# Optimization experiments

Hardware: AMD Instinct MI355X
Metric: run time of the kernel (lower is better)

## Reference

```python
import jax, jax.numpy as jnp
import numpy as np
from jax import lax

BN_EPS = 1e-5
DIST_EPS = 1e-8

def _three_nn_interpolate(xyz1, xyz2, points2):
    # squared pairwise distances: (B, N, S)
    d2 = (jnp.sum(xyz1 ** 2, -1)[:, :, None]
          + jnp.sum(xyz2 ** 2, -1)[:, None, :]
          - 2.0 * jnp.einsum('bnd,bsd->bns', xyz1, xyz2))
    neg_d, idx = lax.top_k(-d2, 3)            # 3 nearest -> (B, N, 3)
    dist = -neg_d
    recip = 1.0 / (dist + DIST_EPS)
    weight = recip / jnp.sum(recip, -1, keepdims=True)   # (B, N, 3)
    gathered = jax.vmap(lambda p, i: p[i])(points2, idx)  # (B, N, 3, C2)
    return jnp.einsum('bnkc,bnk->bnc', gathered, weight)

def _conv_bn_relu(x, w, g, b):
    # x: (B, N, Cin); 1x1 conv == matmul; BatchNorm1d over (B, N) per channel (training stats)
    y = jnp.einsum('bnc,oc->bno', x, w)
    mu = jnp.mean(y, axis=(0, 1))
    var = jnp.mean((y - mu) ** 2, axis=(0, 1))
    yn = (y - mu) * lax.rsqrt(var + BN_EPS)
    return jax.nn.relu(yn * g + b)

def setup_inputs() -> dict:
    key = jax.random.key(0)
    ks = jax.random.split(key, 6)
    B, N, S, C1, C2 = 16, 4096, 1024, 256, 256
    return {
        'xyz1': jax.random.normal(ks[0], (B, N, 3), jnp.float32),
        'xyz2': jax.random.normal(ks[1], (B, S, 3), jnp.float32),
        'points1': jax.random.normal(ks[2], (B, N, C1), jnp.float32),
        'points2': jax.random.normal(ks[3], (B, S, C2), jnp.float32),
        'w1': jax.random.normal(ks[4], (256, C1 + C2), jnp.float32) * 0.04,
        'g1': jnp.ones((256,), jnp.float32),
        'b1': jnp.zeros((256,), jnp.float32),
        'w2': jax.random.normal(ks[5], (256, 256), jnp.float32) * 0.06,
        'g2': jnp.ones((256,), jnp.float32),
        'b2': jnp.zeros((256,), jnp.float32),
    }

def reference(xyz1, xyz2, points1, points2, w1, g1, b1, w2, g2, b2):
    interp = _three_nn_interpolate(xyz1, xyz2, points2)    # (B, N, C2)
    feats = jnp.concatenate([points1, interp], axis=-1)    # (B, N, C1+C2)
    h = _conv_bn_relu(feats, w1, g1, b1)
    out = _conv_bn_relu(h, w2, g2, b2)
    return out                                              # (B, N, 256)
```

## Files before the change

### kernel.cpp

```cpp
#include <hip/hip_runtime.h>
#include <stdint.h>

typedef unsigned short ushort_t;
typedef __bf16 bf16x8 __attribute__((ext_vector_type(8)));
typedef float f32x4 __attribute__((ext_vector_type(4)));
typedef unsigned short ushort8 __attribute__((ext_vector_type(8)));
typedef unsigned short ushort4_t __attribute__((ext_vector_type(4)));

#define DEV static __device__ __forceinline__

DEV unsigned short f2bf(float f) {
    union { float f; unsigned int i; } v; v.f = f;
    unsigned int u = v.i;
    return (unsigned short)((u + 0x7fffu + ((u >> 16) & 1u)) >> 16);
}
DEV float bf2f(unsigned short u) {
    union { unsigned int i; float f; } v; v.i = ((unsigned int)u) << 16; return v.f;
}
DEV bf16x8 u2b(ushort8 u) { union { ushort8 u; bf16x8 b; } x; x.u = u; return x.b; }

__global__ __launch_bounds__(256) void prep_kernel(
    const float* __restrict__ w1, const float* __restrict__ w2,
    const float* __restrict__ points2,
    ushort_t* __restrict__ w1b, ushort_t* __restrict__ w2b,
    ushort_t* __restrict__ p2b, float* __restrict__ stats)
{
    const int bx = blockIdx.x;
    if (bx < 512) {
        int i = bx * 256 + threadIdx.x;
        w1b[i] = f2bf(w1[i]);
    } else if (bx < 768) {
        int i = (bx - 512) * 256 + threadIdx.x;
        w2b[i] = f2bf(w2[i]);
    } else if (bx < 4864) {
        int i = ((bx - 768) * 256 + threadIdx.x) * 4;
        float4 v = *(const float4*)(points2 + i);
        ushort4_t o;
        o[0] = f2bf(v.x); o[1] = f2bf(v.y); o[2] = f2bf(v.z); o[3] = f2bf(v.w);
        *(ushort4_t*)(p2b + i) = o;
    } else {
        int i = threadIdx.x * 8;
        *(float4*)(stats + i)     = make_float4(0.f, 0.f, 0.f, 0.f);
        *(float4*)(stats + i + 4) = make_float4(0.f, 0.f, 0.f, 0.f);
    }
}

__global__ __launch_bounds__(256) void knn_kernel(
    const float* __restrict__ xyz1, const float* __restrict__ xyz2,
    int* __restrict__ idx_out, float* __restrict__ w_out)
{
    __shared__ float4 P[1024];
    __shared__ float mD[24][32];
    __shared__ int   mI[24][32];
    const int b = blockIdx.y;
    const int tid = threadIdx.x;
    for (int s = tid; s < 1024; s += 256) {
        const float* p = xyz2 + ((size_t)b * 1024 + s) * 3;
        float x = p[0], y = p[1], z = p[2];
        float pp = __fadd_rn(__fadd_rn(__fmul_rn(x, x), __fmul_rn(y, y)), __fmul_rn(z, z));
        P[s] = make_float4(x, y, z, pp);
    }
    __syncthreads();
    const int ql = tid & 31;
    const int chunk = tid >> 5;
    const int n = blockIdx.x * 32 + ql;
    const float* q = xyz1 + ((size_t)b * 4096 + n) * 3;
    float qx = q[0], qy = q[1], qz = q[2];
    float qq = __fadd_rn(__fadd_rn(__fmul_rn(qx, qx), __fmul_rn(qy, qy)), __fmul_rn(qz, qz));
    float d0 = 1e30f, d1 = 1e30f, d2 = 1e30f;
    int i0 = 0, i1 = 0, i2 = 0;
    const int s0 = chunk * 128;
#pragma unroll 4
    for (int s = s0; s < s0 + 128; ++s) {
        float4 p = P[s];
        float dot = __fadd_rn(__fadd_rn(__fmul_rn(qx, p.x), __fmul_rn(qy, p.y)), __fmul_rn(qz, p.z));
        float d = __fsub_rn(__fadd_rn(qq, p.w), __fmul_rn(2.0f, dot));
        if (d < d2) {
            if (d < d1) {
                d2 = d1; i2 = i1;
                if (d < d0) { d1 = d0; i1 = i0; d0 = d; i0 = s; }
                else        { d1 = d;  i1 = s; }
            } else { d2 = d; i2 = s; }
        }
    }
    mD[chunk * 3 + 0][ql] = d0; mI[chunk * 3 + 0][ql] = i0;
    mD[chunk * 3 + 1][ql] = d1; mI[chunk * 3 + 1][ql] = i1;
    mD[chunk * 3 + 2][ql] = d2; mI[chunk * 3 + 2][ql] = i2;
    __syncthreads();
    if (tid < 32) {
        float e0 = 1e30f, e1 = 1e30f, e2 = 1e30f;
        int j0 = 0, j1 = 0, j2 = 0;
#pragma unroll
        for (int c = 0; c < 24; ++c) {
            float d = mD[c][ql]; int i = mI[c][ql];
            if (d < e2) {
                if (d < e1) {
                    e2 = e1; j2 = j1;
                    if (d < e0) { e1 = e0; j1 = j0; e0 = d; j0 = i; }
                    else        { e1 = d;  j1 = i; }
                } else { e2 = d; j2 = i; }
            }
        }
        float r0 = 1.0f / (e0 + 1e-8f);
        float r1 = 1.0f / (e1 + 1e-8f);
        float r2 = 1.0f / (e2 + 1e-8f);
        float rs = __fadd_rn(__fadd_rn(r0, r1), r2);
        size_t o = ((size_t)b * 4096 + n) * 3;
        idx_out[o + 0] = j0; idx_out[o + 1] = j1; idx_out[o + 2] = j2;
        w_out[o + 0] = r0 / rs; w_out[o + 1] = r1 / rs; w_out[o + 2] = r2 / rs;
    }
}

DEV void cvt8(const float4& u0, const float4& u1, ushort8& hv) {
    hv[0] = f2bf(u0.x); hv[1] = f2bf(u0.y); hv[2] = f2bf(u0.z); hv[3] = f2bf(u0.w);
    hv[4] = f2bf(u1.x); hv[5] = f2bf(u1.y); hv[6] = f2bf(u1.z); hv[7] = f2bf(u1.w);
}

__global__ __launch_bounds__(1024, 4) void gemm1_kernel(
    const float* __restrict__ p1, const ushort_t* __restrict__ p2b,
    const int* __restrict__ idx, const float* __restrict__ wgt,
    const ushort_t* __restrict__ w1b, ushort_t* __restrict__ y,
    float* __restrict__ sums, float* __restrict__ sqs)
{
    __shared__ __align__(16) char smem[133120];
    ushort_t* Bs = (ushort_t*)smem;
    const int tid = threadIdx.x;
    const int wave = tid >> 6, lane = tid & 63;
    const int frl = lane & 15, fq = lane >> 4;
    const int bid = blockIdx.x;
    const int xcd = bid & 7;
    const int j6 = bid >> 3;
    const int batch = xcd * 2 + (j6 >> 5);
    const int wblk = j6 & 31;
    const int panel = batch * 16 + (wblk >> 1), nb = wblk & 1;
    const int m0 = panel * 256;

    {
        const int c = tid >> 3, qq = tid & 7;
        const ushort_t* src = w1b + (size_t)(nb * 128 + c) * 512;
        ushort_t* dst = Bs + c * 520;
#pragma unroll
        for (int s = 0; s < 8; ++s) {
            int off = qq * 8 + s * 64;
            *(ushort8*)(dst + off) = *(const ushort8*)(src + off);
        }
    }

    f32x4 acc[8];
#pragma unroll
    for (int j = 0; j < 8; ++j) acc[j] = f32x4{0.0f, 0.0f, 0.0f, 0.0f};

    const int row0 = m0 + wave * 16 + frl;
    const size_t io = (size_t)row0 * 3;
    const float iw0 = wgt[io], iw1 = wgt[io + 1], iw2 = wgt[io + 2];
    const ushort_t* pb = p2b + (size_t)(row0 >> 12) * (1024 * 256);
    const ushort_t* gp0 = pb + (size_t)idx[io] * 256 + fq * 8;
    const ushort_t* gp1 = pb + (size_t)idx[io + 1] * 256 + fq * 8;
    const ushort_t* gp2 = pb + (size_t)idx[io + 2] * 256 + fq * 8;

    __syncthreads();

    bf16x8 afb[2], bfb[2][8];

#define G1_LOADA(buf, kc) {                                                        \
    if ((kc) < 8) {                                                                \
        const float4* g = (const float4*)(p1 + (size_t)row0 * 256                  \
                                          + (kc) * 32 + fq * 8);                   \
        float4 u0 = g[0], u1 = g[1];                                               \
        ushort8 hv; cvt8(u0, u1, hv);                                              \
        buf = u2b(hv);                                                             \
    } else {                                                                       \
        ushort8 ga = *(const ushort8*)(gp0 + ((kc) - 8) * 32);                     \
        ushort8 gb = *(const ushort8*)(gp1 + ((kc) - 8) * 32);                     \
        ushort8 gc = *(const ushort8*)(gp2 + ((kc) - 8) * 32);                     \
        ushort8 hv;                                                                \
        _Pragma("unroll")                                                          \
        for (int e = 0; e < 8; ++e) {                                              \
            float av = __fmul_rn(iw0, bf2f(ga[e]));                                \
            av = fmaf(iw1, bf2f(gb[e]), av);                                       \
            av = fmaf(iw2, bf2f(gc[e]), av);                                       \
            hv[e] = f2bf(av);                                                      \
        }                                                                          \
        buf = u2b(hv);                                                             \
    } }
#define G1_LOADB(buf, kc) { _Pragma("unroll")                                      \
    for (int j = 0; j < 8; ++j)                                                    \
        buf[j] = *(const bf16x8*)(Bs + (j * 16 + frl) * 520 + (kc) * 32 + fq * 8); }

    G1_LOADA(afb[0], 0); G1_LOADB(bfb[0], 0);
#pragma unroll
    for (int kc = 0; kc < 16; ++kc) {
        const int cur = kc & 1, nxt = cur ^ 1;
        if (kc < 15) { G1_LOADA(afb[nxt], kc + 1); G1_LOADB(bfb[nxt], kc + 1); }
#pragma unroll
        for (int j = 0; j < 8; ++j)
            acc[j] = __builtin_amdgcn_mfma_f32_16x16x32_bf16(afb[cur], bfb[cur][j], acc[j], 0, 0, 0);
    }

    float ps[8], pq[8];
#pragma unroll
    for (int j = 0; j < 8; ++j) {
        const int colg = nb * 128 + j * 16 + frl;
        float s = 0.f, q = 0.f;
#pragma unroll
        for (int rr = 0; rr < 4; ++rr) {
            ushort_t hb = f2bf(acc[j][rr]);
            float v = bf2f(hb);
            y[(size_t)(m0 + wave * 16 + fq * 4 + rr) * 256 + colg] = hb;
            s += v; q = fmaf(v, v, q);
        }
        s += __shfl_xor(s, 16); s += __shfl_xor(s, 32);
        q += __shfl_xor(q, 16); q += __shfl_xor(q, 32);
        ps[j] = s; pq[j] = q;
    }
    __syncthreads();
    float* scrS = (float*)smem;
    float* scrQ = (float*)(smem + 8192);
    if (fq == 0) {
#pragma unroll
        for (int j = 0; j < 8; ++j) {
            scrS[wave * 128 + j * 16 + frl] = ps[j];
            scrQ[wave * 128 + j * 16 + frl] = pq[j];
        }
    }
    __syncthreads();
    if (tid < 128) {
        float s = 0.f, q = 0.f;
#pragma unroll
        for (int w = 0; w < 16; ++w) { s += scrS[w * 128 + tid]; q += scrQ[w * 128 + tid]; }
        atomicAdd(&sums[nb * 128 + tid], s);
        atomicAdd(&sqs[nb * 128 + tid], q);
    }
}

__global__ __launch_bounds__(512, 2) void gemm2_kernel(
    const ushort_t* __restrict__ y1, const ushort_t* __restrict__ w2b,
    const float* __restrict__ sums1, const float* __restrict__ sqs1,
    const float* __restrict__ g1, const float* __restrict__ b1,
    ushort_t* __restrict__ y2, float* __restrict__ sums, float* __restrict__ sqs)
{
    __shared__ __align__(16) char smem[137216];
    ushort_t* As = (ushort_t*)smem;
    ushort_t* Bs = (ushort_t*)(smem + 67584);
    float* sAv = (float*)(smem + 135168);
    float* sCv = (float*)(smem + 136192);
    const int tid = threadIdx.x;
    const int wave = tid >> 6, lane = tid & 63;
    const int frl = lane & 15, fq = lane >> 4;
    const int panel = blockIdx.x >> 1, nb = blockIdx.x & 1;
    const int m0 = panel * 128;

    if (tid < 256) {
        const float inv_n = 1.0f / 65536.0f;
        float mu = sums1[tid] * inv_n;
        float var = fmaf(-mu, mu, sqs1[tid] * inv_n);
        float is = 1.0f / sqrtf(var + 1e-5f);
        float aa = g1[tid] * is;
        sAv[tid] = aa;
        sCv[tid] = fmaf(-mu, aa, b1[tid]);
    }
    __syncthreads();

    {
        const int r = tid >> 2, qq = tid & 3;
        const ushort_t* srcA = y1 + (size_t)(m0 + r) * 256;
        ushort_t* dstA = As + r * 264;
        const ushort_t* srcB = w2b + (size_t)(nb * 128 + r) * 256;
        ushort_t* dstB = Bs + r * 264;
#pragma unroll
        for (int s = 0; s < 8; ++s) {
            int off = qq * 8 + s * 32;
            ushort8 raw = *(const ushort8*)(srcA + off);
            ushort8 hv;
#pragma unroll
            for (int e = 0; e < 8; ++e) {
                float v = bf2f(raw[e]);
                hv[e] = f2bf(fmaxf(fmaf(v, sAv[off + e], sCv[off + e]), 0.0f));
            }
            *(ushort8*)(dstA + off) = hv;
            *(ushort8*)(dstB + off) = *(const ushort8*)(srcB + off);
        }
    }

    f32x4 acc[2][4];
#pragma unroll
    for (int i = 0; i < 2; ++i)
#pragma unroll
        for (int j = 0; j < 4; ++j) acc[i][j] = f32x4{0.0f, 0.0f, 0.0f, 0.0f};

    __syncthreads();

    const int rg = (wave & 3) * 32, cg = (wave >> 2) * 64;
    bf16x8 afb[2][2], bfb[2][4];

#define G2_LOADA(buf, kc) { _Pragma("unroll")                                      \
    for (int i = 0; i < 2; ++i)                                                    \
        buf[i] = *(const bf16x8*)(As + (rg + i * 16 + frl) * 264 + (kc) * 32 + fq * 8); }
#define G2_LOADB(buf, kc) { _Pragma("unroll")                                      \
    for (int j = 0; j < 4; ++j)                                                    \
        buf[j] = *(const bf16x8*)(Bs + (cg + j * 16 + frl) * 264 + (kc) * 32 + fq * 8); }

    G2_LOADA(afb[0], 0); G2_LOADB(bfb[0], 0);
#pragma unroll
    for (int kc = 0; kc < 8; ++kc) {
        const int cur = kc & 1, nxt = cur ^ 1;
        if (kc < 7) { G2_LOADA(afb[nxt], kc + 1); G2_LOADB(bfb[nxt], kc + 1); }
#pragma unroll
        for (int i = 0; i < 2; ++i)
#pragma unroll
            for (int j = 0; j < 4; ++j)
                acc[i][j] = __builtin_amdgcn_mfma_f32_16x16x32_bf16(afb[cur][i], bfb[cur][j], acc[i][j], 0, 0, 0);
    }

    float ps[4], pq[4];
#pragma unroll
    for (int j = 0; j < 4; ++j) {
        const int colg = nb * 128 + cg + j * 16 + frl;
        float s = 0.f, q = 0.f;
#pragma unroll
        for (int i = 0; i < 2; ++i)
#pragma unroll
            for (int rr = 0; rr < 4; ++rr) {
                ushort_t hb = f2bf(acc[i][j][rr]);
                float v = bf2f(hb);
                y2[(size_t)(m0 + rg + i * 16 + fq * 4 + rr) * 256 + colg] = hb;
                s += v; q = fmaf(v, v, q);
            }
        s += __shfl_xor(s, 16); s += __shfl_xor(s, 32);
        q += __shfl_xor(q, 16); q += __shfl_xor(q, 32);
        ps[j] = s; pq[j] = q;
    }
    __syncthreads();
    float* scrS = (float*)smem;
    float* scrQ = (float*)(smem + 2048);
    if (fq == 0) {
#pragma unroll
        for (int j = 0; j < 4; ++j) {
            scrS[wave * 64 + j * 16 + frl] = ps[j];
            scrQ[wave * 64 + j * 16 + frl] = pq[j];
        }
    }
    __syncthreads();
    if (tid < 128) {
        const int g = tid >> 6, cw = tid & 63;
        float s = 0.f, q = 0.f;
#pragma unroll
        for (int k = 0; k < 4; ++k) {
            s += scrS[(g * 4 + k) * 64 + cw];
            q += scrQ[(g * 4 + k) * 64 + cw];
        }
        atomicAdd(&sums[nb * 128 + g * 64 + cw], s);
        atomicAdd(&sqs[nb * 128 + g * 64 + cw], q);
    }
}

__global__ __launch_bounds__(256) void apply_kernel(
    const ushort_t* __restrict__ y2,
    const float* __restrict__ sums2, const float* __restrict__ sqs2,
    const float* __restrict__ g2, const float* __restrict__ b2,
    float* __restrict__ out)
{
    __shared__ float sA[256], sC[256];
    {
        const int ch2 = threadIdx.x;
        const float inv_n = 1.0f / 65536.0f;
        float mu = sums2[ch2] * inv_n;
        float var = fmaf(-mu, mu, sqs2[ch2] * inv_n);
        float is = 1.0f / sqrtf(var + 1e-5f);
        float aa = g2[ch2] * is;
        sA[ch2] = aa;
        sC[ch2] = fmaf(-mu, aa, b2[ch2]);
    }
    __syncthreads();
    const size_t i = ((size_t)blockIdx.x * 256 + threadIdx.x) * 8;
    const int ch = (int)(i & 255);
    ushort8 raw = *(const ushort8*)(y2 + i);
    float4 o0, o1;
    const float4 a0 = *(const float4*)(sA + ch), a1v = *(const float4*)(sA + ch + 4);
    const float4 c0 = *(const float4*)(sC + ch), c1v = *(const float4*)(sC + ch + 4);
    o0.x = fmaxf(fmaf(bf2f(raw[0]), a0.x, c0.x), 0.0f);
    o0.y = fmaxf(fmaf(bf2f(raw[1]), a0.y, c0.y), 0.0f);
    o0.z = fmaxf(fmaf(bf2f(raw[2]), a0.z, c0.z), 0.0f);
    o0.w = fmaxf(fmaf(bf2f(raw[3]), a0.w, c0.w), 0.0f);
    o1.x = fmaxf(fmaf(bf2f(raw[4]), a1v.x, c1v.x), 0.0f);
    o1.y = fmaxf(fmaf(bf2f(raw[5]), a1v.y, c1v.y), 0.0f);
    o1.z = fmaxf(fmaf(bf2f(raw[6]), a1v.z, c1v.z), 0.0f);
    o1.w = fmaxf(fmaf(bf2f(raw[7]), a1v.w, c1v.w), 0.0f);
    *(float4*)(out + i) = o0;
    *(float4*)(out + i + 4) = o1;
}

extern "C" void kernel_launch(void* const* d_in, const int* in_sizes, int n_in,
                              void* d_out, int out_size, void* d_ws, size_t ws_size,
                              hipStream_t stream)
{
    const float* xyz1    = (const float*)d_in[0];
    const float* xyz2    = (const float*)d_in[1];
    const float* points1 = (const float*)d_in[2];
    const float* points2 = (const float*)d_in[3];
    const float* w1      = (const float*)d_in[4];
    const float* g1      = (const float*)d_in[5];
    const float* b1      = (const float*)d_in[6];
    const float* w2      = (const float*)d_in[7];
    const float* g2      = (const float*)d_in[8];
    const float* b2      = (const float*)d_in[9];
    float* out = (float*)d_out;

    char* ws = (char*)d_ws;
    float* sums1 = (float*)(ws + 0);
    float* sqs1  = (float*)(ws + 1024);
    float* sums2 = (float*)(ws + 4096);
    float* sqs2  = (float*)(ws + 5120);
    ushort_t* w1b = (ushort_t*)(ws + (64u << 10));
    ushort_t* w2b = (ushort_t*)(ws + (320u << 10));
    ushort_t* p2b = (ushort_t*)(ws + (1u << 20));
    int*   idx   = (int*)(ws + (10u << 20));
    float* wgt   = (float*)(ws + (11u << 20));
    ushort_t* y2b = (ushort_t*)(ws + (12u << 20));
    ushort_t* y1  = (ushort_t*)(ws + (44u << 20));

    prep_kernel<<<dim3(4865), 256, 0, stream>>>(w1, w2, points2, w1b, w2b, p2b, (float*)ws);
    knn_kernel<<<dim3(128, 16), 256, 0, stream>>>(xyz1, xyz2, idx, wgt);
    gemm1_kernel<<<dim3(512), 1024, 0, stream>>>(points1, p2b, idx, wgt, w1b, y1, sums1, sqs1);
    gemm2_kernel<<<dim3(1024), 512, 0, stream>>>(y1, w2b, sums1, sqs1, g1, b1, y2b, sums2, sqs2);
    apply_kernel<<<dim3(8192), 256, 0, stream>>>(y2b, sums2, sqs2, g2, b2, out);
}
```

Before: 272.8 us.

## Load gemm2 A operand directly from global into registers, halving LDS footprint

gemm2 no longer stages the normalized y1 tile in shared memory. Each wave now owns 16 rows and all 128 columns, and reads its A fragments straight from global memory, applying BN1+ReLU in registers. Shared memory use drops to about 68KB and the launch bounds hint moves to 4 blocks per CU, aiming at higher occupancy and one fewer staging pass. The cost is that B fragments are now read by every wave for 8 column tiles, and A reads are uncoalesced row slices from global memory.

```diff
diff --git a/kernel.cpp b/kernel.cpp
--- a/kernel.cpp
+++ b/kernel.cpp
@@ -233,17 +233,16 @@
     }
 }
 
-__global__ __launch_bounds__(512, 2) void gemm2_kernel(
+__global__ __launch_bounds__(512, 4) void gemm2_kernel(
     const ushort_t* __restrict__ y1, const ushort_t* __restrict__ w2b,
     const float* __restrict__ sums1, const float* __restrict__ sqs1,
     const float* __restrict__ g1, const float* __restrict__ b1,
     ushort_t* __restrict__ y2, float* __restrict__ sums, float* __restrict__ sqs)
 {
-    __shared__ __align__(16) char smem[137216];
-    ushort_t* As = (ushort_t*)smem;
-    ushort_t* Bs = (ushort_t*)(smem + 67584);
-    float* sAv = (float*)(smem + 135168);
-    float* sCv = (float*)(smem + 136192);
+    __shared__ __align__(16) char smem[69632];
+    ushort_t* Bs = (ushort_t*)smem;
+    float* sAv = (float*)(smem + 67584);
+    float* sCv = (float*)(smem + 68608);
     const int tid = threadIdx.x;
     const int wave = tid >> 6, lane = tid & 63;
     const int frl = lane & 15, fq = lane >> 4;
@@ -259,46 +258,41 @@
         sAv[tid] = aa;
         sCv[tid] = fmaf(-mu, aa, b1[tid]);
     }
-    __syncthreads();
 
     {
-        const int r = tid >> 2, qq = tid & 3;
-        const ushort_t* srcA = y1 + (size_t)(m0 + r) * 256;
-        ushort_t* dstA = As + r * 264;
-        const ushort_t* srcB = w2b + (size_t)(nb * 128 + r) * 256;
-        ushort_t* dstB = Bs + r * 264;
+        const int c = tid >> 2, qq = tid & 3;
+        const ushort_t* src = w2b + (size_t)(nb * 128 + c) * 256;
+        ushort_t* dst = Bs + c * 264;
 #pragma unroll
         for (int s = 0; s < 8; ++s) {
             int off = qq * 8 + s * 32;
-            ushort8 raw = *(const ushort8*)(srcA + off);
-            ushort8 hv;
-#pragma unroll
-            for (int e = 0; e < 8; ++e) {
-                float v = bf2f(raw[e]);
-                hv[e] = f2bf(fmaxf(fmaf(v, sAv[off + e], sCv[off + e]), 0.0f));
-            }
-            *(ushort8*)(dstA + off) = hv;
-            *(ushort8*)(dstB + off) = *(const ushort8*)(srcB + off);
-        }
-    }
-
-    f32x4 acc[2][4];
-#pragma unroll
-    for (int i = 0; i < 2; ++i)
-#pragma unroll
-        for (int j = 0; j < 4; ++j) acc[i][j] = f32x4{0.0f, 0.0f, 0.0f, 0.0f};
-
-    __syncthreads();
-
-    const int rg = (wave & 3) * 32, cg = (wave >> 2) * 64;
-    bf16x8 afb[2][2], bfb[2][4];
-
-#define G2_LOADA(buf, kc) { _Pragma("unroll")                                      \
-    for (int i = 0; i < 2; ++i)                                                    \
-        buf[i] = *(const bf16x8*)(As + (rg + i * 16 + frl) * 264 + (kc) * 32 + fq * 8); }
+            *(ushort8*)(dst + off) = *(const ushort8*)(src + off);
+        }
+    }
+
+    f32x4 acc[8];
+#pragma unroll
+    for (int j = 0; j < 8; ++j) acc[j] = f32x4{0.0f, 0.0f, 0.0f, 0.0f};
+
+    const int row0 = m0 + wave * 16 + frl;
+
+    __syncthreads();
+
+    bf16x8 afb[2], bfb[2][8];
+
+#define G2_LOADA(buf, kc) {                                                        \
+    ushort8 raw = *(const ushort8*)(y1 + (size_t)row0 * 256 + (kc) * 32 + fq * 8); \
+    ushort8 hv;                                                                    \
+    _Pragma("unroll")                                                              \
+    for (int e = 0; e < 8; ++e) {                                                  \
+        const int kk = (kc) * 32 + fq * 8 + e;                                     \
+        float v = bf2f(raw[e]);                                                    \
+        hv[e] = f2bf(fmaxf(fmaf(v, sAv[kk], sCv[kk]), 0.0f));                      \
+    }                                                                              \
+    buf = u2b(hv); }
 #define G2_LOADB(buf, kc) { _Pragma("unroll")                                      \
-    for (int j = 0; j < 4; ++j)                                                    \
-        buf[j] = *(const bf16x8*)(Bs + (cg + j * 16 + frl) * 264 + (kc) * 32 + fq * 8); }
+    for (int j = 0; j < 8; ++j)                                                    \
+        buf[j] = *(const bf16x8*)(Bs + (j * 16 + frl) * 264 + (kc) * 32 + fq * 8); }
 
     G2_LOADA(afb[0], 0); G2_LOADB(bfb[0], 0);
 #pragma unroll
@@ -306,51 +300,43 @@
         const int cur = kc & 1, nxt = cur ^ 1;
         if (kc < 7) { G2_LOADA(afb[nxt], kc + 1); G2_LOADB(bfb[nxt], kc + 1); }
 #pragma unroll
-        for (int i = 0; i < 2; ++i)
-#pragma unroll
-            for (int j = 0; j < 4; ++j)
-                acc[i][j] = __builtin_amdgcn_mfma_f32_16x16x32_bf16(afb[cur][i], bfb[cur][j], acc[i][j], 0, 0, 0);
-    }
-
-    float ps[4], pq[4];
-#pragma unroll
-    for (int j = 0; j < 4; ++j) {
-        const int colg = nb * 128 + cg + j * 16 + frl;
+        for (int j = 0; j < 8; ++j)
+            acc[j] = __builtin_amdgcn_mfma_f32_16x16x32_bf16(afb[cur], bfb[cur][j], acc[j], 0, 0, 0);
+    }
+
+    float ps[8], pq[8];
+#pragma unroll
+    for (int j = 0; j < 8; ++j) {
+        const int colg = nb * 128 + j * 16 + frl;
         float s = 0.f, q = 0.f;
 #pragma unroll
-        for (int i = 0; i < 2; ++i)
-#pragma unroll
-            for (int rr = 0; rr < 4; ++rr) {
-                ushort_t hb = f2bf(acc[i][j][rr]);
-                float v = bf2f(hb);
-                y2[(size_t)(m0 + rg + i * 16 + fq * 4 + rr) * 256 + colg] = hb;
-                s += v; q = fmaf(v, v, q);
-            }
+        for (int rr = 0; rr < 4; ++rr) {
+            ushort_t hb = f2bf(acc[j][rr]);
+            float v = bf2f(hb);
+            y2[(size_t)(m0 + wave * 16 + fq * 4 + rr) * 256 + colg] = hb;
+            s += v; q = fmaf(v, v, q);
+        }
         s += __shfl_xor(s, 16); s += __shfl_xor(s, 32);
         q += __shfl_xor(q, 16); q += __shfl_xor(q, 32);
         ps[j] = s; pq[j] = q;
     }
     __syncthreads();
     float* scrS = (float*)smem;
-    float* scrQ = (float*)(smem + 2048);
+    float* scrQ = (float*)(smem + 4096);
     if (fq == 0) {
 #pragma unroll
-        for (int j = 0; j < 4; ++j) {
-            scrS[wave * 64 + j * 16 + frl] = ps[j];
-            scrQ[wave * 64 + j * 16 + frl] = pq[j];
+        for (int j = 0; j < 8; ++j) {
+            scrS[wave * 128 + j * 16 + frl] = ps[j];
+            scrQ[wave * 128 + j * 16 + frl] = pq[j];
         }
     }
     __syncthreads();
     if (tid < 128) {
-        const int g = tid >> 6, cw = tid & 63;
         float s = 0.f, q = 0.f;
 #pragma unroll
-        for (int k = 0; k < 4; ++k) {
-            s += scrS[(g * 4 + k) * 64 + cw];
-            q += scrQ[(g * 4 + k) * 64 + cw];
-        }
-        atomicAdd(&sums[nb * 128 + g * 64 + cw], s);
-        atomicAdd(&sqs[nb * 128 + g * 64 + cw], q);
+        for (int w = 0; w < 8; ++w) { s += scrS[w * 128 + tid]; q += scrQ[w * 128 + tid]; }
+        atomicAdd(&sums[nb * 128 + tid], s);
+        atomicAdd(&sqs[nb * 128 + tid], q);
     }
 }
 
```

Result: no change. 268.7 us (-1.5%).
